# Optimization experiments

Hardware: AMD Instinct MI355X
Metric: run time of the kernel (lower is better)

Reference implementation:

```python
import math
import jax, jax.numpy as jnp
import numpy as np

B, S, IN = 2, 2048, 2048
HID, H = 2048, 16
D = HID // H  # 128, dim_per_head


def setup_inputs() -> dict:
    key = jax.random.key(0)
    k1, k2, k3, k4 = jax.random.split(key, 4)
    x = jax.random.normal(k1, (B, S, IN), dtype=jnp.float32)
    # nn.Linear(input_size, hidden_size, bias=False) weights: [out, in]
    w_scale = 0.02
    Wq = jax.random.normal(k2, (HID, IN), dtype=jnp.float32) * w_scale
    Wk = jax.random.normal(k3, (HID, IN), dtype=jnp.float32) * w_scale
    Wv = jax.random.normal(k4, (HID, IN), dtype=jnp.float32) * w_scale
    return {"x": x, "Wq": Wq, "Wk": Wk, "Wv": Wv}


def reference(x, Wq, Wk, Wv):
    b, s, _ = x.shape
    scale = 1.0 / math.sqrt(D)
    # query projection over all query chunks at once (chunking is a pure reshape)
    q = (x @ Wq.T) * scale              # [b, s, hid]
    q = q.reshape(b, s, H, D)           # flattened query chunks: bqhd
    # key/value projections; the python loop over 64 kv chunks is just a
    # partition of the seq axis, so computing all chunks at once is identical
    k = (x @ Wk.T).reshape(b, s, H, D)  # bkhd
    v = (x @ Wv.T).reshape(b, s, H, D)  # computed then discarded by the module
    # per-chunk einsum 'bqhd,bkhd->bqhk' concatenated over kv chunks == full scores
    attn_weights = jnp.einsum('bqhd,bkhd->bqhk', q, k)  # [b, s, H, s]
    # the original module discards all of the above and returns zeros
    attn_output = jnp.zeros((b, s, HID), dtype=x.dtype)
    return attn_output, attn_weights
```

## Files before the change

kernel.cpp:

```cpp
#include <hip/hip_runtime.h>
#include <hip/hip_bf16.h>
#include <cstdint>
#include <cmath>

typedef __bf16 bf16_t;
typedef __attribute__((ext_vector_type(8))) bf16_t bf16x8;
typedef __attribute__((ext_vector_type(4))) float f32x4;

#define AS_GLOBAL(p) ((const __attribute__((address_space(1))) void*)(p))
#define AS_LDS(p)    ((__attribute__((address_space(3))) void*)(p))

__device__ __forceinline__ unsigned short f2bf(float f) {
  unsigned u = __builtin_bit_cast(unsigned, f);
  u += 0x7FFFu + ((u >> 16) & 1u);
  return (unsigned short)(u >> 16);
}

#define N4_X  2097152
#define N4_W  1048576
__global__ void cvt3_kernel(const float* __restrict__ x, const float* __restrict__ wq,
                            const float* __restrict__ wk, ushort4* __restrict__ xb4,
                            ushort4* __restrict__ wb4, float scale) {
  int i = blockIdx.x * blockDim.x + threadIdx.x;
  int stride = gridDim.x * blockDim.x;
  for (; i < N4_X + 2 * N4_W; i += stride) {
    const float4* src;
    ushort4* dst;
    float sc = 1.0f;
    if (i < N4_X) {
      src = reinterpret_cast<const float4*>(x) + i;
      dst = xb4 + i;
    } else if (i < N4_X + N4_W) {
      src = reinterpret_cast<const float4*>(wq) + (i - N4_X);
      dst = wb4 + (i - N4_X);
      sc = scale;
    } else {
      src = reinterpret_cast<const float4*>(wk) + (i - N4_X - N4_W);
      dst = wb4 + (i - N4_X);
    }
    float4 v = *src;
    ushort4 o;
    o.x = f2bf(v.x * sc);
    o.y = f2bf(v.y * sc);
    o.z = f2bf(v.z * sc);
    o.w = f2bf(v.w * sc);
    *dst = o;
  }
}

#define PM 4096
#define PN 4096
#define PK 2048

__global__ __launch_bounds__(256) void proj_gemm(const unsigned short* __restrict__ A,
                                                 const unsigned short* __restrict__ Bm,
                                                 unsigned short* __restrict__ C) {
  __shared__ unsigned short As[128 * 64];
  __shared__ unsigned short Bs[128 * 64];
  const int tid = threadIdx.x;
  const int wave = tid >> 6, lane = tid & 63;
  const int m0 = blockIdx.y * 128;
  const int n0 = blockIdx.x * 128;
  const int wr = wave >> 1, wc = wave & 1;

  f32x4 acc[4][4] = {};

  for (int kt = 0; kt < PK; kt += 64) {
    #pragma unroll
    for (int j = 0; j < 4; ++j) {
      int base = (wave * 4 + j) * 1024;
      int o = base + lane * 16;
      int row = o >> 7;
      int c = o & 127;
      int csrc = c ^ ((row & 7) << 4);
      const char* ga = (const char*)(A + (size_t)(m0 + row) * PK + kt) + csrc;
      __builtin_amdgcn_global_load_lds(AS_GLOBAL(ga), AS_LDS((char*)As + base), 16, 0, 0);
      const char* gb = (const char*)(Bm + (size_t)(n0 + row) * PK + kt) + csrc;
      __builtin_amdgcn_global_load_lds(AS_GLOBAL(gb), AS_LDS((char*)Bs + base), 16, 0, 0);
    }
    __syncthreads();

    #pragma unroll
    for (int ks = 0; ks < 2; ++ks) {
      bf16x8 av[4], bv[4];
      const int kbyte = ks * 64 + (lane >> 4) * 16;
      #pragma unroll
      for (int i = 0; i < 4; ++i) {
        int row = wr * 64 + i * 16 + (lane & 15);
        int off = row * 128 + (kbyte ^ ((row & 7) << 4));
        av[i] = *(const bf16x8*)((const char*)As + off);
      }
      #pragma unroll
      for (int j = 0; j < 4; ++j) {
        int row = wc * 64 + j * 16 + (lane & 15);
        int off = row * 128 + (kbyte ^ ((row & 7) << 4));
        bv[j] = *(const bf16x8*)((const char*)Bs + off);
      }
      #pragma unroll
      for (int i = 0; i < 4; ++i)
        #pragma unroll
        for (int j = 0; j < 4; ++j)
          acc[i][j] = __builtin_amdgcn_mfma_f32_16x16x32_bf16(av[i], bv[j], acc[i][j], 0, 0, 0);
    }
    __syncthreads();
  }

  #pragma unroll
  for (int i = 0; i < 4; ++i)
    #pragma unroll
    for (int j = 0; j < 4; ++j)
      #pragma unroll
      for (int r = 0; r < 4; ++r) {
        int row = m0 + wr * 64 + i * 16 + (lane >> 4) * 4 + r;
        int col = n0 + wc * 64 + j * 16 + (lane & 15);
        C[(size_t)row * PN + col] = f2bf(acc[i][j][r]);
      }
}

__global__ __launch_bounds__(256) void scores_kernel(const unsigned short* __restrict__ qk,
                                                     float* __restrict__ out2) {
  __shared__ unsigned short Ks[2][128 * 128];
  const int tid = threadIdx.x;
  const int wave = tid >> 6, lane = tid & 63;
  const int qtile = blockIdx.x;
  const int bh = blockIdx.y;
  const int b = bh >> 4, h = bh & 15;
  const int wr = wave >> 1, wc = wave & 1;

  const unsigned short* qbase = qk + (size_t)(b * 2048 + qtile * 128) * 4096 + h * 128;
  const unsigned short* kbase = qk + (size_t)(b * 2048) * 4096 + 2048 + h * 128;

  bf16x8 qv[4][4];
  #pragma unroll
  for (int i = 0; i < 4; ++i) {
    int row = wr * 64 + i * 16 + (lane & 15);
    const unsigned short* qr = qbase + (size_t)row * 4096 + (lane >> 4) * 8;
    #pragma unroll
    for (int ks = 0; ks < 4; ++ks)
      qv[i][ks] = *(const bf16x8*)(qr + ks * 32);
  }

  auto stageK = [&](int bi, int kt) {
    const unsigned short* kb = kbase + (size_t)kt * 128 * 4096;
    #pragma unroll
    for (int j = 0; j < 8; ++j) {
      int base = (wave * 8 + j) * 1024;
      int o = base + lane * 16;
      int row = o >> 8;
      int c = o & 255;
      int csrc = c ^ ((row & 7) << 4);
      const char* gk = (const char*)(kb + (size_t)row * 4096) + csrc;
      __builtin_amdgcn_global_load_lds(AS_GLOBAL(gk), AS_LDS((char*)Ks[bi] + base), 16, 0, 0);
    }
  };

  float* obase = out2 + ((size_t)(b * 2048 + qtile * 128) * 16 + h) * 2048;
  const size_t qstride = (size_t)16 * 2048;

  stageK(0, 0);
  __syncthreads();

  int cur = 0;
  for (int kt = 0; kt < 16; ++kt) {
    if (kt + 1 < 16) stageK(cur ^ 1, kt + 1);

    f32x4 acc[4][4] = {};
    #pragma unroll
    for (int ks = 0; ks < 4; ++ks) {
      bf16x8 bv[4];
      const int kbyte = ks * 64 + (lane >> 4) * 16;
      #pragma unroll
      for (int j = 0; j < 4; ++j) {
        int row = wc * 64 + j * 16 + (lane & 15);
        int off = row * 256 + (kbyte ^ ((row & 7) << 4));
        bv[j] = *(const bf16x8*)((const char*)Ks[cur] + off);
      }
      #pragma unroll
      for (int i = 0; i < 4; ++i)
        #pragma unroll
        for (int j = 0; j < 4; ++j)
          acc[i][j] = __builtin_amdgcn_mfma_f32_16x16x32_bf16(qv[i][ks], bv[j], acc[i][j], 0, 0, 0);
    }

    __syncthreads();

    #pragma unroll
    for (int i = 0; i < 4; ++i)
      #pragma unroll
      for (int j = 0; j < 4; ++j)
        #pragma unroll
        for (int r = 0; r < 4; ++r) {
          int qrow = wr * 64 + i * 16 + (lane >> 4) * 4 + r;
          int col = kt * 128 + wc * 64 + j * 16 + (lane & 15);
          obase[(size_t)qrow * qstride + col] = acc[i][j][r];
        }

    cur ^= 1;
  }
}

extern "C" void kernel_launch(void* const* d_in, const int* in_sizes, int n_in,
                              void* d_out, int out_size, void* d_ws, size_t ws_size,
                              hipStream_t stream) {
  const float* x  = (const float*)d_in[0];
  const float* Wq = (const float*)d_in[1];
  const float* Wk = (const float*)d_in[2];

  float* out = (float*)d_out;
  unsigned short* xb = (unsigned short*)d_ws;
  unsigned short* wb = xb + (size_t)4096 * 2048;
  unsigned short* qkbuf = wb + (size_t)4096 * 2048;

  const float scale = 1.0f / sqrtf(128.0f);

  hipMemsetAsync(d_out, 0, (size_t)2 * 2048 * 2048 * sizeof(float), stream);

  cvt3_kernel<<<2048, 256, 0, stream>>>(x, Wq, Wk, (ushort4*)xb, (ushort4*)wb, scale);

  proj_gemm<<<dim3(PN / 128, PM / 128), 256, 0, stream>>>(xb, wb, qkbuf);

  scores_kernel<<<dim3(16, 32), 256, 0, stream>>>(qkbuf, out + (size_t)2 * 2048 * 2048);
}
```

Measured before the change: 251.2 us.

## Rewrite projection GEMM with 256x256 tiles and phased async-load pipeline

Replaces the 128x128-tile projection GEMM with a 512-thread, 256x256-tile kernel. It double-buffers 128KB of LDS and splits each K-step into four quadrant phases. Each phase issues the next half-tile global-to-LDS loads ahead of time, waits with explicit vmcnt thresholds, and raises wave priority around the MFMA bursts. The aim is to hide load latency and raise arithmetic intensity per block. In exchange, the grid shrinks to 256 blocks with heavy LDS use per block, and correctness now depends on hand-tuned waitcnt counts.

```diff
diff --git a/kernel.cpp b/kernel.cpp
--- a/kernel.cpp
+++ b/kernel.cpp
@@ -51,70 +51,134 @@
 #define PM 4096
 #define PN 4096
 #define PK 2048
-
-__global__ __launch_bounds__(256) void proj_gemm(const unsigned short* __restrict__ A,
-                                                 const unsigned short* __restrict__ Bm,
-                                                 unsigned short* __restrict__ C) {
-  __shared__ unsigned short As[128 * 64];
-  __shared__ unsigned short Bs[128 * 64];
+#define PNT 32
+
+template<int VM> __device__ __forceinline__ void waitcnt_vm() {
+  if constexpr (VM == 0)  asm volatile("s_waitcnt vmcnt(0)" ::: "memory");
+  else if constexpr (VM == 2)  asm volatile("s_waitcnt vmcnt(2)" ::: "memory");
+  else if constexpr (VM == 4)  asm volatile("s_waitcnt vmcnt(4)" ::: "memory");
+  else if constexpr (VM == 6)  asm volatile("s_waitcnt vmcnt(6)" ::: "memory");
+  else if constexpr (VM == 8)  asm volatile("s_waitcnt vmcnt(8)" ::: "memory");
+  else if constexpr (VM == 10) asm volatile("s_waitcnt vmcnt(10)" ::: "memory");
+}
+
+__device__ __forceinline__ void stage_half(const unsigned short* A, const unsigned short* B,
+                                           int m0, int n0, int H, int wave, int lane,
+                                           char* lds) {
+  int tile = H >> 2;
+  int mat  = H & 1;
+  int half = (H >> 1) & 1;
+  int buf  = tile & 1;
+  const unsigned short* src = mat ? B : A;
+  int base0 = mat ? n0 : m0;
+  char* hbase = lds + (((buf * 2 + mat) * 2 + half) * 16384);
+  #pragma unroll
+  for (int l = 0; l < 2; ++l) {
+    int o = l * 8192 + wave * 1024 + lane * 16;
+    int row = o >> 7;
+    int c = o & 127;
+    int csrc = c ^ ((row & 7) << 4);
+    const char* g = (const char*)(src + (size_t)(base0 + half * 128 + row) * PK)
+                    + tile * 128 + csrc;
+    __builtin_amdgcn_global_load_lds(AS_GLOBAL(g), AS_LDS(hbase + l * 8192 + wave * 1024),
+                                     16, 0, 0);
+  }
+}
+
+template<int Q, int VM>
+__device__ __forceinline__ void phase(const unsigned short* A, const unsigned short* B,
+                                      int m0, int n0, int T, int wave, int lane,
+                                      int wm, int wn, char* lds, f32x4 (&acc)[8][4]) {
+  constexpr int gm = Q >> 1, gn = Q & 1;
+  const int buf = T & 1;
+  const char* Ab = lds + (((buf * 2 + 0) * 2 + gm) * 16384);
+  const char* Bb = lds + (((buf * 2 + 1) * 2 + gn) * 16384);
+
+  bf16x8 av[4][2], bv[2][2];
+  #pragma unroll
+  for (int j = 0; j < 4; ++j) {
+    int row = j * 32 + wm * 16 + (lane & 15);
+    #pragma unroll
+    for (int ks = 0; ks < 2; ++ks) {
+      int kb = ks * 64 + (lane >> 4) * 16;
+      av[j][ks] = *(const bf16x8*)(Ab + row * 128 + (kb ^ ((row & 7) << 4)));
+    }
+  }
+  #pragma unroll
+  for (int i = 0; i < 2; ++i) {
+    int row = i * 64 + wn * 16 + (lane & 15);
+    #pragma unroll
+    for (int ks = 0; ks < 2; ++ks) {
+      int kb = ks * 64 + (lane >> 4) * 16;
+      bv[i][ks] = *(const bf16x8*)(Bb + row * 128 + (kb ^ ((row & 7) << 4)));
+    }
+  }
+
+  int H = 4 * T + Q + 6;
+  if (H < 4 * PNT) stage_half(A, B, m0, n0, H, wave, lane, lds);
+
+  waitcnt_vm<VM>();
+  asm volatile("s_barrier" ::: "memory");
+  asm volatile("s_waitcnt lgkmcnt(0)" ::: "memory");
+  __builtin_amdgcn_sched_barrier(0);
+
+  __builtin_amdgcn_s_setprio(1);
+  #pragma unroll
+  for (int j = 0; j < 4; ++j)
+    #pragma unroll
+    for (int i = 0; i < 2; ++i)
+      #pragma unroll
+      for (int ks = 0; ks < 2; ++ks)
+        acc[gm * 4 + j][gn * 2 + i] =
+          __builtin_amdgcn_mfma_f32_16x16x32_bf16(av[j][ks], bv[i][ks],
+                                                  acc[gm * 4 + j][gn * 2 + i], 0, 0, 0);
+  __builtin_amdgcn_s_setprio(0);
+  asm volatile("s_barrier" ::: "memory");
+}
+
+__global__ __launch_bounds__(512, 2) void proj_gemm(const unsigned short* __restrict__ A,
+                                                    const unsigned short* __restrict__ Bm,
+                                                    unsigned short* __restrict__ C) {
+  __shared__ __align__(16) char lds[131072];
   const int tid = threadIdx.x;
   const int wave = tid >> 6, lane = tid & 63;
-  const int m0 = blockIdx.y * 128;
-  const int n0 = blockIdx.x * 128;
-  const int wr = wave >> 1, wc = wave & 1;
-
-  f32x4 acc[4][4] = {};
-
-  for (int kt = 0; kt < PK; kt += 64) {
-    #pragma unroll
-    for (int j = 0; j < 4; ++j) {
-      int base = (wave * 4 + j) * 1024;
-      int o = base + lane * 16;
-      int row = o >> 7;
-      int c = o & 127;
-      int csrc = c ^ ((row & 7) << 4);
-      const char* ga = (const char*)(A + (size_t)(m0 + row) * PK + kt) + csrc;
-      __builtin_amdgcn_global_load_lds(AS_GLOBAL(ga), AS_LDS((char*)As + base), 16, 0, 0);
-      const char* gb = (const char*)(Bm + (size_t)(n0 + row) * PK + kt) + csrc;
-      __builtin_amdgcn_global_load_lds(AS_GLOBAL(gb), AS_LDS((char*)Bs + base), 16, 0, 0);
-    }
-    __syncthreads();
-
-    #pragma unroll
-    for (int ks = 0; ks < 2; ++ks) {
-      bf16x8 av[4], bv[4];
-      const int kbyte = ks * 64 + (lane >> 4) * 16;
-      #pragma unroll
-      for (int i = 0; i < 4; ++i) {
-        int row = wr * 64 + i * 16 + (lane & 15);
-        int off = row * 128 + (kbyte ^ ((row & 7) << 4));
-        av[i] = *(const bf16x8*)((const char*)As + off);
-      }
-      #pragma unroll
-      for (int j = 0; j < 4; ++j) {
-        int row = wc * 64 + j * 16 + (lane & 15);
-        int off = row * 128 + (kbyte ^ ((row & 7) << 4));
-        bv[j] = *(const bf16x8*)((const char*)Bs + off);
-      }
-      #pragma unroll
-      for (int i = 0; i < 4; ++i)
-        #pragma unroll
-        for (int j = 0; j < 4; ++j)
-          acc[i][j] = __builtin_amdgcn_mfma_f32_16x16x32_bf16(av[i], bv[j], acc[i][j], 0, 0, 0);
-    }
-    __syncthreads();
-  }
-
-  #pragma unroll
-  for (int i = 0; i < 4; ++i)
-    #pragma unroll
-    for (int j = 0; j < 4; ++j)
-      #pragma unroll
-      for (int r = 0; r < 4; ++r) {
-        int row = m0 + wr * 64 + i * 16 + (lane >> 4) * 4 + r;
-        int col = n0 + wc * 64 + j * 16 + (lane & 15);
-        C[(size_t)row * PN + col] = f2bf(acc[i][j][r]);
-      }
+  const int wm = wave >> 2, wn = wave & 3;
+  const int m0 = blockIdx.y * 256;
+  const int n0 = blockIdx.x * 256;
+
+  f32x4 acc[8][4] = {};
+
+  #pragma unroll
+  for (int h = 0; h < 6; ++h) stage_half(A, Bm, m0, n0, h, wave, lane, lds);
+  waitcnt_vm<8>();
+  asm volatile("s_barrier" ::: "memory");
+
+  for (int T = 0; T < PNT - 2; ++T) {
+    phase<0, 6>(A, Bm, m0, n0, T, wave, lane, wm, wn, lds, acc);
+    phase<1, 10>(A, Bm, m0, n0, T, wave, lane, wm, wn, lds, acc);
+    phase<2, 10>(A, Bm, m0, n0, T, wave, lane, wm, wn, lds, acc);
+    phase<3, 8>(A, Bm, m0, n0, T, wave, lane, wm, wn, lds, acc);
+  }
+  phase<0, 6>(A, Bm, m0, n0, PNT - 2, wave, lane, wm, wn, lds, acc);
+  phase<1, 10>(A, Bm, m0, n0, PNT - 2, wave, lane, wm, wn, lds, acc);
+  phase<2, 8>(A, Bm, m0, n0, PNT - 2, wave, lane, wm, wn, lds, acc);
+  phase<3, 4>(A, Bm, m0, n0, PNT - 2, wave, lane, wm, wn, lds, acc);
+  phase<0, 0>(A, Bm, m0, n0, PNT - 1, wave, lane, wm, wn, lds, acc);
+  phase<1, -1>(A, Bm, m0, n0, PNT - 1, wave, lane, wm, wn, lds, acc);
+  phase<2, -1>(A, Bm, m0, n0, PNT - 1, wave, lane, wm, wn, lds, acc);
+  phase<3, -1>(A, Bm, m0, n0, PNT - 1, wave, lane, wm, wn, lds, acc);
+
+  #pragma unroll
+  for (int f = 0; f < 8; ++f) {
+    int rbase = m0 + (f >> 2) * 128 + (f & 3) * 32 + wm * 16 + (lane >> 4) * 4;
+    #pragma unroll
+    for (int nf = 0; nf < 4; ++nf) {
+      int col = n0 + (nf >> 1) * 128 + (nf & 1) * 64 + wn * 16 + (lane & 15);
+      #pragma unroll
+      for (int r = 0; r < 4; ++r)
+        C[(size_t)(rbase + r) * PN + col] = f2bf(acc[f][nf][r]);
+    }
+  }
 }
 
 __global__ __launch_bounds__(256) void scores_kernel(const unsigned short* __restrict__ qk,
@@ -217,7 +281,7 @@
 
   cvt3_kernel<<<2048, 256, 0, stream>>>(x, Wq, Wk, (ushort4*)xb, (ushort4*)wb, scale);
 
-  proj_gemm<<<dim3(PN / 128, PM / 128), 256, 0, stream>>>(xb, wb, qkbuf);
+  proj_gemm<<<dim3(PN / 256, PM / 256), 512, 0, stream>>>(xb, wb, qkbuf);
 
   scores_kernel<<<dim3(16, 32), 256, 0, stream>>>(qkbuf, out + (size_t)2 * 2048 * 2048);
 }
```

Result: faster. 232.0 us (-7.7%).
